# Kernel tuning notes

Measured on AMD Instinct MI355X. Metric: run time of the kernel, lower is better.

The kernel has to match this reference:

```python
import jax, jax.numpy as jnp
import numpy as np

N_NODES = 100000
N_EDGES = 1600000
IN_DIM = 128
HID = 128
OUT_DIM = 64
NLP_DIM = 786  # 768 + 11 + 4 + 3
N_LAYERS = 3
N_USERS = 4096
BN_EPS = 1e-5


def setup_inputs() -> dict:
    key = jax.random.key(0)
    ks = jax.random.split(key, 24)
    inp = {
        "x": jax.random.normal(ks[0], (N_NODES, IN_DIM), jnp.float32),
        "nlp_features": jax.random.normal(ks[1], (NLP_DIM,), jnp.float32),
        "edge_index": jax.random.randint(ks[2], (2, N_EDGES), 0, N_NODES),
        "user_indices": jax.random.randint(ks[3], (N_USERS,), 0, N_NODES),
        # input projection
        "W_in": jax.random.normal(ks[4], (IN_DIM, HID), jnp.float32) / np.sqrt(IN_DIM),
        "b_in": jnp.zeros((HID,), jnp.float32),
        # GCN layers (stacked)
        "W_gnn": jax.random.normal(ks[5], (N_LAYERS, HID, HID), jnp.float32) / np.sqrt(HID),
        "b_gnn": jnp.zeros((N_LAYERS, HID), jnp.float32),
        # batchnorm running stats / affine (eval mode)
        "bn_gamma": jnp.ones((N_LAYERS, HID), jnp.float32),
        "bn_beta": jnp.zeros((N_LAYERS, HID), jnp.float32),
        "bn_mean": 0.1 * jax.random.normal(ks[6], (N_LAYERS, HID), jnp.float32),
        "bn_var": 0.5 + jax.random.uniform(ks[7], (N_LAYERS, HID), jnp.float32),
        # node embedding projection
        "W_proj": jax.random.normal(ks[8], (HID, OUT_DIM), jnp.float32) / np.sqrt(HID),
        "b_proj": jnp.zeros((OUT_DIM,), jnp.float32),
        # predictor MLP
        "W1": jax.random.normal(ks[9], (OUT_DIM + NLP_DIM, 256), jnp.float32) / np.sqrt(OUT_DIM + NLP_DIM),
        "b1": jnp.zeros((256,), jnp.float32),
        "W2": jax.random.normal(ks[10], (256, 128), jnp.float32) / np.sqrt(256.0),
        "b2": jnp.zeros((128,), jnp.float32),
        "W3": jax.random.normal(ks[11], (128, 1), jnp.float32) / np.sqrt(128.0),
        "b3": jnp.zeros((1,), jnp.float32),
    }
    return inp


def reference(x, nlp_features, edge_index, user_indices,
              W_in, b_in, W_gnn, b_gnn, bn_gamma, bn_beta, bn_mean, bn_var,
              W_proj, b_proj, W1, b1, W2, b2, W3, b3):
    n = x.shape[0]
    src, dst = edge_index[0], edge_index[1]
    # GCN normalization with self-loops: deg = in-degree + 1
    deg = jax.ops.segment_sum(jnp.ones_like(src, dtype=x.dtype), dst, num_segments=n) + 1.0
    dinv = jax.lax.rsqrt(deg)                      # [N]
    enorm = dinv[src] * dinv[dst]                  # [E]

    h = jax.nn.relu(x @ W_in + b_in)               # [N, HID]
    for i in range(W_gnn.shape[0]):
        hw = h @ W_gnn[i]                          # [N, HID]
        agg = jax.ops.segment_sum(enorm[:, None] * hw[src], dst, num_segments=n)
        agg = agg + (dinv * dinv)[:, None] * hw + b_gnn[i]  # self-loop + bias
        # batchnorm (eval: running stats) + relu; dropout is identity in eval
        hn = (agg - bn_mean[i]) * jax.lax.rsqrt(bn_var[i] + BN_EPS) * bn_gamma[i] + bn_beta[i]
        h = jax.nn.relu(hn)

    emb = h @ W_proj + b_proj                      # [N, OUT_DIM]
    u = emb[user_indices]                          # [B, OUT_DIM]
    nlp = jnp.broadcast_to(nlp_features, (u.shape[0], nlp_features.shape[0]))
    z = jnp.concatenate([u, nlp], axis=1)          # [B, OUT_DIM+NLP_DIM]
    z = jax.nn.relu(z @ W1 + b1)
    z = jax.nn.relu(z @ W2 + b2)
    probs = jax.nn.sigmoid(z @ W3 + b3)
    return probs.squeeze(-1)
```

## Files before the change

kernel.cpp:

```cpp
#include <hip/hip_runtime.h>
#include <math.h>

typedef _Float16 half8_t __attribute__((ext_vector_type(8)));
typedef _Float16 half4_t __attribute__((ext_vector_type(4)));
typedef float    f32x4_t __attribute__((ext_vector_type(4)));


__global__ __launch_bounds__(256) void hist_k(const int* __restrict__ dst, int* __restrict__ cnt,
                                              int* __restrict__ rank, int E){
  int e = blockIdx.x*256 + threadIdx.x;
  if (e < E) rank[e] = atomicAdd(&cnt[dst[e]], 1);
}

__global__ __launch_bounds__(256) void blocksum_k(const int* __restrict__ cnt, int* __restrict__ bsum, int N){
  int i = blockIdx.x*256 + threadIdx.x;
  int v = (i < N) ? cnt[i] : 0;
  #pragma unroll
  for (int off = 32; off; off >>= 1) v += __shfl_down(v, off, 64);
  __shared__ int s[4];
  if ((threadIdx.x & 63) == 0) s[threadIdx.x >> 6] = v;
  __syncthreads();
  if (threadIdx.x == 0) bsum[blockIdx.x] = s[0] + s[1] + s[2] + s[3];
}

__global__ __launch_bounds__(512) void scan_small_k(const int* __restrict__ bsum, int* __restrict__ boff, int NB){
  __shared__ int s[512];
  int t = threadIdx.x;
  int v = (t < NB) ? bsum[t] : 0;
  s[t] = v; __syncthreads();
  for (int off = 1; off < 512; off <<= 1){
    int x = (t >= off) ? s[t-off] : 0;
    __syncthreads();
    s[t] += x;
    __syncthreads();
  }
  if (t < NB) boff[t] = s[t] - v;
}

__global__ __launch_bounds__(256) void scan_final_k(const int* __restrict__ cnt, const int* __restrict__ boff,
                                                    int* __restrict__ rowptr,
                                                    float* __restrict__ dinv, int N){
  __shared__ int s[256];
  int t = threadIdx.x;
  int i = blockIdx.x*256 + t;
  int v = (i < N) ? cnt[i] : 0;
  s[t] = v; __syncthreads();
  for (int off = 1; off < 256; off <<= 1){
    int x = (t >= off) ? s[t-off] : 0;
    __syncthreads();
    s[t] += x;
    __syncthreads();
  }
  int excl = s[t] - v + boff[blockIdx.x];
  if (i < N){
    rowptr[i] = excl;
    dinv[i]   = rsqrtf((float)v + 1.0f);
    if (i == N-1) rowptr[N] = excl + v;
  }
}

__global__ __launch_bounds__(256) void fill_k(const int* __restrict__ src, const int* __restrict__ dst,
                                              const int* __restrict__ rowptr, const int* __restrict__ rank,
                                              int* __restrict__ col, int E){
  int e = blockIdx.x*256 + threadIdx.x;
  if (e >= E) return;
  col[rowptr[dst[e]] + rank[e]] = src[e];
}


__global__ __launch_bounds__(256) void prepw_k(const float* __restrict__ Win, const float* __restrict__ Wgnn,
                                               _Float16* __restrict__ Bt){
  int idx = blockIdx.x*256 + threadIdx.x;
  int m = idx >> 14;
  int r = idx & 16383;
  int k = r >> 7, n = r & 127;
  const float* W = (m == 0) ? Win : (Wgnn + (size_t)(m-1)*16384);
  Bt[(size_t)m*16384 + n*128 + k] = (_Float16)W[k*128 + n];
}


template<int AF16, int EPI>
__global__ __launch_bounds__(256) void mgemm_k(const void* __restrict__ Ap, const _Float16* __restrict__ Bt,
                                               const float* __restrict__ bias, const float* __restrict__ dinv,
                                               _Float16* __restrict__ C, int M){
  __shared__ _Float16 As[128*128];
  __shared__ _Float16 Bs[128*128];
  const int tid = threadIdx.x;
  const int m0 = blockIdx.x * 128;

  {
    int n = tid >> 1, kb = (tid & 1) * 64;
    const half8_t* srcb = (const half8_t*)(Bt + n*128 + kb);
    #pragma unroll
    for (int q = 0; q < 8; ++q){
      uint32_t byte = (uint32_t)(n*256 + kb*2 + q*16) ^ (uint32_t)((n & 7) << 4);
      *(half8_t*)((char*)Bs + byte) = srcb[q];
    }
  }
  {
    int rr = tid >> 1, kb = (tid & 1) * 64;
    int row = m0 + rr; if (row >= M) row = M - 1;
    if (AF16){
      const half8_t* srca = (const half8_t*)((const _Float16*)Ap + (size_t)row*128 + kb);
      #pragma unroll
      for (int q = 0; q < 8; ++q){
        uint32_t byte = (uint32_t)(rr*256 + kb*2 + q*16) ^ (uint32_t)((rr & 7) << 4);
        *(half8_t*)((char*)As + byte) = srca[q];
      }
    } else {
      const float4* srca = (const float4*)((const float*)Ap + (size_t)row*128 + kb);
      #pragma unroll
      for (int q = 0; q < 8; ++q){
        float4 f0 = srca[2*q], f1 = srca[2*q+1];
        half8_t h;
        h[0]=(_Float16)f0.x; h[1]=(_Float16)f0.y; h[2]=(_Float16)f0.z; h[3]=(_Float16)f0.w;
        h[4]=(_Float16)f1.x; h[5]=(_Float16)f1.y; h[6]=(_Float16)f1.z; h[7]=(_Float16)f1.w;
        uint32_t byte = (uint32_t)(rr*256 + kb*2 + q*16) ^ (uint32_t)((rr & 7) << 4);
        *(half8_t*)((char*)As + byte) = h;
      }
    }
  }
  __syncthreads();

  const int w = tid >> 6, lane = tid & 63;
  const int l15 = lane & 15, lq = lane >> 4;

  f32x4_t acc[2][8];
  #pragma unroll
  for (int rg = 0; rg < 2; ++rg)
    #pragma unroll
    for (int cg = 0; cg < 8; ++cg)
      acc[rg][cg] = (f32x4_t){0.f,0.f,0.f,0.f};

  #pragma unroll
  for (int ks = 0; ks < 4; ++ks){
    half8_t a[2], b[8];
    #pragma unroll
    for (int rg = 0; rg < 2; ++rg){
      int row = w*32 + rg*16 + l15;
      uint32_t byte = (uint32_t)(row*256 + (ks*32 + lq*8)*2) ^ (uint32_t)((row & 7) << 4);
      a[rg] = *(const half8_t*)((const char*)As + byte);
    }
    #pragma unroll
    for (int cg = 0; cg < 8; ++cg){
      int coln = cg*16 + l15;
      uint32_t byte = (uint32_t)(coln*256 + (ks*32 + lq*8)*2) ^ (uint32_t)((coln & 7) << 4);
      b[cg] = *(const half8_t*)((const char*)Bs + byte);
    }
    #pragma unroll
    for (int rg = 0; rg < 2; ++rg)
      #pragma unroll
      for (int cg = 0; cg < 8; ++cg)
        acc[rg][cg] = __builtin_amdgcn_mfma_f32_16x16x32_f16(a[rg], b[cg], acc[rg][cg], 0, 0, 0);
  }

  float bl[8];
  if (EPI == 0){
    #pragma unroll
    for (int cg = 0; cg < 8; ++cg) bl[cg] = bias[cg*16 + l15];
  }

  #pragma unroll
  for (int rg = 0; rg < 2; ++rg){
    #pragma unroll
    for (int r = 0; r < 4; ++r){
      int grow = m0 + w*32 + rg*16 + lq*4 + r;
      if (grow < M){
        if (EPI == 1){
          float di = dinv[grow];
          #pragma unroll
          for (int cg = 0; cg < 8; ++cg)
            C[(size_t)grow*128 + cg*16 + l15] = (_Float16)(di * acc[rg][cg][r]);
        } else {
          #pragma unroll
          for (int cg = 0; cg < 8; ++cg){
            float v = acc[rg][cg][r] + bl[cg];
            C[(size_t)grow*128 + cg*16 + l15] = (_Float16)fmaxf(v, 0.f);
          }
        }
      }
    }
  }
}


template<int ACT>
__global__ __launch_bounds__(256) void gemm_k(const float* __restrict__ A, const float* __restrict__ B,
                                              const float* __restrict__ bias, float* __restrict__ C,
                                              int M, int N, int K){
  __shared__ float As[16][68];
  __shared__ float Bs[16][68];
  int tid = threadIdx.x;
  int m0 = blockIdx.x * 64, n0 = blockIdx.y * 64;
  int ty = tid >> 4, tx = tid & 15;
  int lm = tid >> 2, lkq = tid & 3;
  int lk = tid >> 4, ln4 = tid & 15;
  int arow = m0 + lm; if (arow >= M) arow = M - 1;

  float acc[4][4] = {{0.f}};

  for (int k0 = 0; k0 < K; k0 += 16){
    float4 av = *(const float4*)&A[(size_t)arow*K + k0 + lkq*4];
    float4 bv = *(const float4*)&B[(size_t)(k0+lk)*N + n0 + ln4*4];
    As[lkq*4+0][lm] = av.x; As[lkq*4+1][lm] = av.y; As[lkq*4+2][lm] = av.z; As[lkq*4+3][lm] = av.w;
    *(float4*)&Bs[lk][ln4*4] = bv;
    __syncthreads();
    #pragma unroll
    for (int kk = 0; kk < 16; ++kk){
      const float4 a = *(const float4*)&As[kk][ty*4];
      const float4 b = *(const float4*)&Bs[kk][tx*4];
      acc[0][0] += a.x*b.x; acc[0][1] += a.x*b.y; acc[0][2] += a.x*b.z; acc[0][3] += a.x*b.w;
      acc[1][0] += a.y*b.x; acc[1][1] += a.y*b.y; acc[1][2] += a.y*b.z; acc[1][3] += a.y*b.w;
      acc[2][0] += a.z*b.x; acc[2][1] += a.z*b.y; acc[2][2] += a.z*b.z; acc[2][3] += a.z*b.w;
      acc[3][0] += a.w*b.x; acc[3][1] += a.w*b.y; acc[3][2] += a.w*b.z; acc[3][3] += a.w*b.w;
    }
    __syncthreads();
  }

  float bv0 = 0.f, bv1 = 0.f, bv2 = 0.f, bv3 = 0.f;
  if (bias){
    const float4 b4 = *(const float4*)&bias[n0 + tx*4];
    bv0 = b4.x; bv1 = b4.y; bv2 = b4.z; bv3 = b4.w;
  }
  #pragma unroll
  for (int i = 0; i < 4; ++i){
    int r = m0 + ty*4 + i;
    if (r < M){
      float4 o;
      o.x = acc[i][0] + bv0; o.y = acc[i][1] + bv1; o.z = acc[i][2] + bv2; o.w = acc[i][3] + bv3;
      if (ACT == 1){ o.x = fmaxf(o.x,0.f); o.y = fmaxf(o.y,0.f); o.z = fmaxf(o.z,0.f); o.w = fmaxf(o.w,0.f); }
      *(float4*)&C[(size_t)r*N + n0 + tx*4] = o;
    }
  }
}


__global__ __launch_bounds__(256) void agg_k(const _Float16* __restrict__ hws, _Float16* __restrict__ hout,
                                             const int* __restrict__ rowptr, const int* __restrict__ col,
                                             const float* __restrict__ dinv,
                                             const float* __restrict__ bgnn, const float* __restrict__ gamma,
                                             const float* __restrict__ beta, const float* __restrict__ mean,
                                             const float* __restrict__ var, int N){
  int n = (blockIdx.x * blockDim.x + threadIdx.x) >> 6;
  if (n >= N) return;
  int lane = threadIdx.x & 63;
  int half = lane >> 5;
  int sl   = lane & 31;
  int f    = sl * 4;
  int beg = rowptr[n], end = rowptr[n+1];

  half4_t H0 = {0,0,0,0}, H1 = {0,0,0,0}, H2 = {0,0,0,0}, H3 = {0,0,0,0};

  int j = beg + half;
  for (; j + 6 < end; j += 8){
    int s0 = col[j], s1 = col[j+2], s2 = col[j+4], s3 = col[j+6];
    H0 += *(const half4_t*)&hws[(size_t)s0*128 + f];
    H1 += *(const half4_t*)&hws[(size_t)s1*128 + f];
    H2 += *(const half4_t*)&hws[(size_t)s2*128 + f];
    H3 += *(const half4_t*)&hws[(size_t)s3*128 + f];
  }
  for (; j < end; j += 2){
    int s0 = col[j];
    H0 += *(const half4_t*)&hws[(size_t)s0*128 + f];
  }

  float4 A0;
  A0.x = (float)H0[0] + (float)H1[0] + (float)H2[0] + (float)H3[0];
  A0.y = (float)H0[1] + (float)H1[1] + (float)H2[1] + (float)H3[1];
  A0.z = (float)H0[2] + (float)H1[2] + (float)H2[2] + (float)H3[2];
  A0.w = (float)H0[3] + (float)H1[3] + (float)H2[3] + (float)H3[3];

  A0.x += __shfl_xor(A0.x, 32, 64);
  A0.y += __shfl_xor(A0.y, 32, 64);
  A0.z += __shfl_xor(A0.z, 32, 64);
  A0.w += __shfl_xor(A0.w, 32, 64);

  if (half == 0){
    float di = dinv[n];
    const half4_t hv = *(const half4_t*)&hws[(size_t)n*128 + f];
    const float4 bg = *(const float4*)&bgnn[f];
    const float4 gm = *(const float4*)&gamma[f];
    const float4 bt = *(const float4*)&beta[f];
    const float4 mn = *(const float4*)&mean[f];
    const float4 vr = *(const float4*)&var[f];
    float o0 = (di*(A0.x + (float)hv[0]) + bg.x - mn.x) * (gm.x * rsqrtf(vr.x + 1e-5f)) + bt.x;
    float o1 = (di*(A0.y + (float)hv[1]) + bg.y - mn.y) * (gm.y * rsqrtf(vr.y + 1e-5f)) + bt.y;
    float o2 = (di*(A0.z + (float)hv[2]) + bg.z - mn.z) * (gm.z * rsqrtf(vr.z + 1e-5f)) + bt.z;
    float o3 = (di*(A0.w + (float)hv[3]) + bg.w - mn.w) * (gm.w * rsqrtf(vr.w + 1e-5f)) + bt.w;
    half4_t o;
    o[0] = (_Float16)fmaxf(o0, 0.f);
    o[1] = (_Float16)fmaxf(o1, 0.f);
    o[2] = (_Float16)fmaxf(o2, 0.f);
    o[3] = (_Float16)fmaxf(o3, 0.f);
    *(half4_t*)&hout[(size_t)n*128 + f] = o;
  }
}


__global__ __launch_bounds__(256) void gather_k(const _Float16* __restrict__ h, const int* __restrict__ uidx,
                                                float* __restrict__ uh, int B){
  int g = blockIdx.x*256 + threadIdx.x;
  if (g >= B*128) return;
  int i = g >> 7, f = g & 127;
  uh[g] = (float)h[(size_t)uidx[i]*128 + f];
}

__global__ __launch_bounds__(256) void initc1_k(const float* __restrict__ b1, float* __restrict__ c1){
  c1[threadIdx.x] = b1[threadIdx.x];
}

__global__ __launch_bounds__(256) void c1acc_k(const float* __restrict__ nlp, const float* __restrict__ W1,
                                               float* __restrict__ c1, int NLP){
  int b = blockIdx.x;
  int c  = (b & 3) * 64 + (threadIdx.x & 63);
  int dq = threadIdx.x >> 6;
  int d0 = (b >> 2) * 99;
  float acc = 0.f;
  for (int d = d0 + dq; d < d0 + 99 && d < NLP; d += 4)
    acc += nlp[d] * W1[(size_t)(64 + d) * 256 + c];
  __shared__ float s[256];
  s[threadIdx.x] = acc; __syncthreads();
  if (dq == 0){
    float t = s[threadIdx.x] + s[threadIdx.x + 64] + s[threadIdx.x + 128] + s[threadIdx.x + 192];
    atomicAdd(&c1[c], t);
  }
}

__global__ __launch_bounds__(256) void head_k(const float* __restrict__ z2, const float* __restrict__ W3,
                                              const float* __restrict__ b3, float* __restrict__ out, int B){
  int gid = blockIdx.x * blockDim.x + threadIdx.x;
  int u = gid >> 6, l = gid & 63;
  if (u >= B) return;
  float v = z2[(size_t)u*128 + l] * W3[l] + z2[(size_t)u*128 + 64 + l] * W3[64 + l];
  #pragma unroll
  for (int off = 32; off; off >>= 1) v += __shfl_down(v, off, 64);
  if (l == 0) out[u] = 1.f / (1.f + expf(-(v + b3[0])));
}


static void launch_gemm(int act, const float* A, const float* Bm, const float* bias, float* C,
                        int M, int N, int K, hipStream_t s){
  dim3 g((M + 63) / 64, N / 64);
  if (act) hipLaunchKernelGGL((gemm_k<1>), g, dim3(256), 0, s, A, Bm, bias, C, M, N, K);
  else     hipLaunchKernelGGL((gemm_k<0>), g, dim3(256), 0, s, A, Bm, bias, C, M, N, K);
}

extern "C" void kernel_launch(void* const* d_in, const int* in_sizes, int n_in,
                              void* d_out, int out_size, void* d_ws, size_t ws_size,
                              hipStream_t stream){
  const float* x     = (const float*)d_in[0];
  const float* nlp   = (const float*)d_in[1];
  const int*   eidx  = (const int*)  d_in[2];
  const int*   uidx  = (const int*)  d_in[3];
  const float* W_in  = (const float*)d_in[4];
  const float* b_in  = (const float*)d_in[5];
  const float* W_gnn = (const float*)d_in[6];
  const float* b_gnn = (const float*)d_in[7];
  const float* gam   = (const float*)d_in[8];
  const float* bet   = (const float*)d_in[9];
  const float* mean  = (const float*)d_in[10];
  const float* var   = (const float*)d_in[11];
  const float* Wproj = (const float*)d_in[12];
  const float* bproj = (const float*)d_in[13];
  const float* W1    = (const float*)d_in[14];
  const float* b1    = (const float*)d_in[15];
  const float* W2    = (const float*)d_in[16];
  const float* b2    = (const float*)d_in[17];
  const float* W3    = (const float*)d_in[18];
  const float* b3    = (const float*)d_in[19];
  float* out = (float*)d_out;

  const int N   = in_sizes[0] / 128;
  const int E   = in_sizes[2] / 2;
  const int B   = in_sizes[3];
  const int NLP = in_sizes[1];
  const int HID = 128;

  char* p = (char*)d_ws;
  auto carve = [&](size_t bytes) -> void* {
    void* q = (void*)p;
    p += (bytes + 255) & ~(size_t)255;
    return q;
  };
  int*      cnt    = (int*)     carve((size_t)N * 4);
  int*      rowptr = (int*)     carve((size_t)(N + 1) * 4);
  int*      rank   = (int*)     carve((size_t)E * 4);
  int*      bsum   = (int*)     carve(512 * 4);
  int*      boff   = (int*)     carve(512 * 4);
  float*    dinv   = (float*)   carve((size_t)N * 4);
  int*      col    = (int*)     carve((size_t)E * 4);
  _Float16* Bt     = (_Float16*)carve((size_t)4 * 128 * 128 * 2);
  _Float16* h      = (_Float16*)carve((size_t)N * HID * 2);
  _Float16* hws    = (_Float16*)carve((size_t)N * HID * 2);
  float*    uh     = (float*)   carve((size_t)B * HID * 4);
  float*    embu   = (float*)   carve((size_t)B * 64 * 4);
  float*    z1     = (float*)   carve((size_t)B * 256 * 4);
  float*    z2     = (float*)   carve((size_t)B * 128 * 4);
  float*    c1     = (float*)   carve(256 * 4);

  const int* src = eidx;
  const int* dst = eidx + E;

  const int NB = (N + 255) / 256;
  const int GB = (N + 127) / 128;

  hipMemsetAsync(cnt, 0, (size_t)N * 4, stream);
  hipLaunchKernelGGL(hist_k, dim3((E + 255) / 256), dim3(256), 0, stream, dst, cnt, rank, E);
  hipLaunchKernelGGL(blocksum_k, dim3(NB), dim3(256), 0, stream, cnt, bsum, N);
  hipLaunchKernelGGL(scan_small_k, dim3(1), dim3(512), 0, stream, bsum, boff, NB);
  hipLaunchKernelGGL(scan_final_k, dim3(NB), dim3(256), 0, stream, cnt, boff, rowptr, dinv, N);
  hipLaunchKernelGGL(fill_k, dim3((E + 255) / 256), dim3(256), 0, stream, src, dst, rowptr, rank, col, E);

  hipLaunchKernelGGL(prepw_k, dim3(256), dim3(256), 0, stream, W_in, W_gnn, Bt);

  hipLaunchKernelGGL((mgemm_k<0,0>), dim3(GB), dim3(256), 0, stream,
                     (const void*)x, Bt, b_in, (const float*)nullptr, h, N);

  for (int i = 0; i < 3; ++i){
    hipLaunchKernelGGL((mgemm_k<1,1>), dim3(GB), dim3(256), 0, stream,
                       (const void*)h, Bt + (size_t)(i+1)*16384, (const float*)nullptr, dinv, hws, N);
    hipLaunchKernelGGL(agg_k, dim3((N * 64 + 255) / 256), dim3(256), 0, stream,
                       hws, h, rowptr, col, dinv,
                       b_gnn + i * 128, gam + i * 128, bet + i * 128, mean + i * 128, var + i * 128, N);
  }

  hipLaunchKernelGGL(gather_k, dim3((B * 128 + 255) / 256), dim3(256), 0, stream, h, uidx, uh, B);
  hipLaunchKernelGGL(initc1_k, dim3(1), dim3(256), 0, stream, b1, c1);
  hipLaunchKernelGGL(c1acc_k, dim3(32), dim3(256), 0, stream, nlp, W1, c1, NLP);

  launch_gemm(0, uh, Wproj, bproj, embu, B, 64, 128, stream);
  launch_gemm(1, embu, W1, c1, z1, B, 256, 64, stream);
  launch_gemm(1, z1, W2, b2, z2, B, 128, 256, stream);
  hipLaunchKernelGGL(head_k, dim3((B * 64 + 255) / 256), dim3(256), 0, stream, z2, W3, b3, out, B);
}
```

Measured before the change: 567.5 us.

## Shrink rank to u16, vectorize fill, unroll aggregation to 8 accumulators, merge c1 kernels

Edge ranks are stored as 16-bit values, halving that buffer's traffic, and the CSR fill kernel now processes two edges per thread with vector loads. The GCN aggregation loop is unrolled to eight independent half4 accumulators so more neighbour gathers are in flight per thread. The NLP bias precompute is merged into one kernel without atomics. The 16-bit rank is only correct while every in-degree stays below 65536, and the extra accumulators raise register pressure.

```diff
diff --git a/kernel.cpp b/kernel.cpp
--- a/kernel.cpp
+++ b/kernel.cpp
@@ -7,9 +7,9 @@
 
 
 __global__ __launch_bounds__(256) void hist_k(const int* __restrict__ dst, int* __restrict__ cnt,
-                                              int* __restrict__ rank, int E){
+                                              unsigned short* __restrict__ rank, int E){
   int e = blockIdx.x*256 + threadIdx.x;
-  if (e < E) rank[e] = atomicAdd(&cnt[dst[e]], 1);
+  if (e < E) rank[e] = (unsigned short)atomicAdd(&cnt[dst[e]], 1);
 }
 
 __global__ __launch_bounds__(256) void blocksum_k(const int* __restrict__ cnt, int* __restrict__ bsum, int N){
@@ -60,11 +60,16 @@
 }
 
 __global__ __launch_bounds__(256) void fill_k(const int* __restrict__ src, const int* __restrict__ dst,
-                                              const int* __restrict__ rowptr, const int* __restrict__ rank,
+                                              const int* __restrict__ rowptr,
+                                              const unsigned short* __restrict__ rank,
                                               int* __restrict__ col, int E){
-  int e = blockIdx.x*256 + threadIdx.x;
-  if (e >= E) return;
-  col[rowptr[dst[e]] + rank[e]] = src[e];
+  int e2 = (blockIdx.x*256 + threadIdx.x) * 2;
+  if (e2 >= E) return;
+  int2 d = *(const int2*)&dst[e2];
+  int2 s = *(const int2*)&src[e2];
+  ushort2 r = *(const ushort2*)&rank[e2];
+  col[rowptr[d.x] + r.x] = s.x;
+  col[rowptr[d.y] + r.y] = s.y;
 }
 
 
@@ -248,27 +253,45 @@
   int sl   = lane & 31;
   int f    = sl * 4;
   int beg = rowptr[n], end = rowptr[n+1];
+  const _Float16* hwsf = hws + f;
 
   half4_t H0 = {0,0,0,0}, H1 = {0,0,0,0}, H2 = {0,0,0,0}, H3 = {0,0,0,0};
+  half4_t H4 = {0,0,0,0}, H5 = {0,0,0,0}, H6 = {0,0,0,0}, H7 = {0,0,0,0};
 
   int j = beg + half;
+  for (; j + 14 < end; j += 16){
+    int s0 = col[j],    s1 = col[j+2],  s2 = col[j+4],  s3 = col[j+6];
+    int s4 = col[j+8],  s5 = col[j+10], s6 = col[j+12], s7 = col[j+14];
+    H0 += *(const half4_t*)&hwsf[(size_t)s0*128];
+    H1 += *(const half4_t*)&hwsf[(size_t)s1*128];
+    H2 += *(const half4_t*)&hwsf[(size_t)s2*128];
+    H3 += *(const half4_t*)&hwsf[(size_t)s3*128];
+    H4 += *(const half4_t*)&hwsf[(size_t)s4*128];
+    H5 += *(const half4_t*)&hwsf[(size_t)s5*128];
+    H6 += *(const half4_t*)&hwsf[(size_t)s6*128];
+    H7 += *(const half4_t*)&hwsf[(size_t)s7*128];
+  }
   for (; j + 6 < end; j += 8){
     int s0 = col[j], s1 = col[j+2], s2 = col[j+4], s3 = col[j+6];
-    H0 += *(const half4_t*)&hws[(size_t)s0*128 + f];
-    H1 += *(const half4_t*)&hws[(size_t)s1*128 + f];
-    H2 += *(const half4_t*)&hws[(size_t)s2*128 + f];
-    H3 += *(const half4_t*)&hws[(size_t)s3*128 + f];
+    H0 += *(const half4_t*)&hwsf[(size_t)s0*128];
+    H1 += *(const half4_t*)&hwsf[(size_t)s1*128];
+    H2 += *(const half4_t*)&hwsf[(size_t)s2*128];
+    H3 += *(const half4_t*)&hwsf[(size_t)s3*128];
   }
   for (; j < end; j += 2){
     int s0 = col[j];
-    H0 += *(const half4_t*)&hws[(size_t)s0*128 + f];
+    H0 += *(const half4_t*)&hwsf[(size_t)s0*128];
   }
 
   float4 A0;
-  A0.x = (float)H0[0] + (float)H1[0] + (float)H2[0] + (float)H3[0];
-  A0.y = (float)H0[1] + (float)H1[1] + (float)H2[1] + (float)H3[1];
-  A0.z = (float)H0[2] + (float)H1[2] + (float)H2[2] + (float)H3[2];
-  A0.w = (float)H0[3] + (float)H1[3] + (float)H2[3] + (float)H3[3];
+  A0.x = ((float)H0[0] + (float)H1[0]) + ((float)H2[0] + (float)H3[0])
+       + ((float)H4[0] + (float)H5[0]) + ((float)H6[0] + (float)H7[0]);
+  A0.y = ((float)H0[1] + (float)H1[1]) + ((float)H2[1] + (float)H3[1])
+       + ((float)H4[1] + (float)H5[1]) + ((float)H6[1] + (float)H7[1]);
+  A0.z = ((float)H0[2] + (float)H1[2]) + ((float)H2[2] + (float)H3[2])
+       + ((float)H4[2] + (float)H5[2]) + ((float)H6[2] + (float)H7[2]);
+  A0.w = ((float)H0[3] + (float)H1[3]) + ((float)H2[3] + (float)H3[3])
+       + ((float)H4[3] + (float)H5[3]) + ((float)H6[3] + (float)H7[3]);
 
   A0.x += __shfl_xor(A0.x, 32, 64);
   A0.y += __shfl_xor(A0.y, 32, 64);
@@ -277,7 +300,7 @@
 
   if (half == 0){
     float di = dinv[n];
-    const half4_t hv = *(const half4_t*)&hws[(size_t)n*128 + f];
+    const half4_t hv = *(const half4_t*)&hwsf[(size_t)n*128];
     const float4 bg = *(const float4*)&bgnn[f];
     const float4 gm = *(const float4*)&gamma[f];
     const float4 bt = *(const float4*)&beta[f];
@@ -305,25 +328,17 @@
   uh[g] = (float)h[(size_t)uidx[i]*128 + f];
 }
 
-__global__ __launch_bounds__(256) void initc1_k(const float* __restrict__ b1, float* __restrict__ c1){
-  c1[threadIdx.x] = b1[threadIdx.x];
-}
-
-__global__ __launch_bounds__(256) void c1acc_k(const float* __restrict__ nlp, const float* __restrict__ W1,
-                                               float* __restrict__ c1, int NLP){
-  int b = blockIdx.x;
-  int c  = (b & 3) * 64 + (threadIdx.x & 63);
+__global__ __launch_bounds__(256) void c1_k(const float* __restrict__ nlp, const float* __restrict__ W1,
+                                            const float* __restrict__ b1, float* __restrict__ c1, int NLP){
+  int c  = blockIdx.x * 64 + (threadIdx.x & 63);
   int dq = threadIdx.x >> 6;
-  int d0 = (b >> 2) * 99;
   float acc = 0.f;
-  for (int d = d0 + dq; d < d0 + 99 && d < NLP; d += 4)
+  for (int d = dq; d < NLP; d += 4)
     acc += nlp[d] * W1[(size_t)(64 + d) * 256 + c];
   __shared__ float s[256];
   s[threadIdx.x] = acc; __syncthreads();
-  if (dq == 0){
-    float t = s[threadIdx.x] + s[threadIdx.x + 64] + s[threadIdx.x + 128] + s[threadIdx.x + 192];
-    atomicAdd(&c1[c], t);
-  }
+  if (dq == 0)
+    c1[c] = b1[c] + s[threadIdx.x] + s[threadIdx.x + 64] + s[threadIdx.x + 128] + s[threadIdx.x + 192];
 }
 
 __global__ __launch_bounds__(256) void head_k(const float* __restrict__ z2, const float* __restrict__ W3,
@@ -382,21 +397,21 @@
     p += (bytes + 255) & ~(size_t)255;
     return q;
   };
-  int*      cnt    = (int*)     carve((size_t)N * 4);
-  int*      rowptr = (int*)     carve((size_t)(N + 1) * 4);
-  int*      rank   = (int*)     carve((size_t)E * 4);
-  int*      bsum   = (int*)     carve(512 * 4);
-  int*      boff   = (int*)     carve(512 * 4);
-  float*    dinv   = (float*)   carve((size_t)N * 4);
-  int*      col    = (int*)     carve((size_t)E * 4);
-  _Float16* Bt     = (_Float16*)carve((size_t)4 * 128 * 128 * 2);
-  _Float16* h      = (_Float16*)carve((size_t)N * HID * 2);
-  _Float16* hws    = (_Float16*)carve((size_t)N * HID * 2);
-  float*    uh     = (float*)   carve((size_t)B * HID * 4);
-  float*    embu   = (float*)   carve((size_t)B * 64 * 4);
-  float*    z1     = (float*)   carve((size_t)B * 256 * 4);
-  float*    z2     = (float*)   carve((size_t)B * 128 * 4);
-  float*    c1     = (float*)   carve(256 * 4);
+  int*            cnt    = (int*)           carve((size_t)N * 4);
+  int*            rowptr = (int*)           carve((size_t)(N + 1) * 4);
+  unsigned short* rank   = (unsigned short*)carve((size_t)E * 2);
+  int*            bsum   = (int*)           carve(512 * 4);
+  int*            boff   = (int*)           carve(512 * 4);
+  float*          dinv   = (float*)         carve((size_t)N * 4);
+  int*            col    = (int*)           carve((size_t)E * 4);
+  _Float16*       Bt     = (_Float16*)      carve((size_t)4 * 128 * 128 * 2);
+  _Float16*       h      = (_Float16*)      carve((size_t)N * HID * 2);
+  _Float16*       hws    = (_Float16*)      carve((size_t)N * HID * 2);
+  float*          uh     = (float*)         carve((size_t)B * HID * 4);
+  float*          embu   = (float*)         carve((size_t)B * 64 * 4);
+  float*          z1     = (float*)         carve((size_t)B * 256 * 4);
+  float*          z2     = (float*)         carve((size_t)B * 128 * 4);
+  float*          c1     = (float*)         carve(256 * 4);
 
   const int* src = eidx;
   const int* dst = eidx + E;
@@ -409,7 +424,7 @@
   hipLaunchKernelGGL(blocksum_k, dim3(NB), dim3(256), 0, stream, cnt, bsum, N);
   hipLaunchKernelGGL(scan_small_k, dim3(1), dim3(512), 0, stream, bsum, boff, NB);
   hipLaunchKernelGGL(scan_final_k, dim3(NB), dim3(256), 0, stream, cnt, boff, rowptr, dinv, N);
-  hipLaunchKernelGGL(fill_k, dim3((E + 255) / 256), dim3(256), 0, stream, src, dst, rowptr, rank, col, E);
+  hipLaunchKernelGGL(fill_k, dim3((E/2 + 255) / 256), dim3(256), 0, stream, src, dst, rowptr, rank, col, E);
 
   hipLaunchKernelGGL(prepw_k, dim3(256), dim3(256), 0, stream, W_in, W_gnn, Bt);
 
@@ -425,8 +440,7 @@
   }
 
   hipLaunchKernelGGL(gather_k, dim3((B * 128 + 255) / 256), dim3(256), 0, stream, h, uidx, uh, B);
-  hipLaunchKernelGGL(initc1_k, dim3(1), dim3(256), 0, stream, b1, c1);
-  hipLaunchKernelGGL(c1acc_k, dim3(32), dim3(256), 0, stream, nlp, W1, c1, NLP);
+  hipLaunchKernelGGL(c1_k, dim3(4), dim3(256), 0, stream, nlp, W1, b1, c1, NLP);
 
   launch_gemm(0, uh, Wproj, bproj, embu, B, 64, 128, stream);
   launch_gemm(1, embu, W1, c1, z1, B, 256, 64, stream);
```

After: 603.7 us. 1.06x slower.
